# Kernel tuning notes

Hardware: AMD Instinct MI355X
Metric: run time of the kernel (lower is better)

Reference implementation:

```python
import jax, jax.numpy as jnp
import numpy as np

K = 64  # hardcoded in MAN.__init__
D_DRUG = 128
D_PROT = 128


def setup_inputs() -> dict:
    key = jax.random.key(0)
    ks = jax.random.split(key, 7)
    B, Ld, Lp = 64, 512, 1024

    def xavier(k, shape):
        fan_in, fan_out = shape[-1], shape[-2]
        std = (2.0 / (fan_in + fan_out)) ** 0.5
        return jax.random.normal(k, shape, dtype=jnp.float32) * std

    return {
        "drug": jax.random.normal(ks[0], (B, Ld, D_DRUG), dtype=jnp.float32),
        "target": jax.random.normal(ks[1], (B, Lp, D_PROT), dtype=jnp.float32),
        "W_b": xavier(ks[2], (D_PROT, D_DRUG)),
        "W_x": xavier(ks[3], (K, D_DRUG)),
        "W_p": xavier(ks[4], (K, D_PROT)),
        "w_hx": xavier(ks[5], (K, 1)),
        "w_hp": xavier(ks[6], (K, 1)),
    }


def reference(drug, target, W_b, W_x, W_p, w_hx, w_hp):
    # drug:   [B, Ld, Dd] ; target: [B, Lp, Dp]
    d = jnp.swapaxes(drug, 1, 2)            # [B, Dd, Ld]  (drug.permute(0,2,1))
    tT = jnp.swapaxes(target, 1, 2)         # [B, Dp, Lp]

    # C = tanh(target @ (W_b @ d))  -> [B, Lp, Ld]
    C = jnp.tanh(jnp.einsum('bpe,ed,bdl->bpl', target, W_b, d))

    Wx_d = jnp.einsum('kd,bdl->bkl', W_x, d)     # [B, k, Ld]
    Wp_t = jnp.einsum('ke,bep->bkp', W_p, tT)    # [B, k, Lp]

    H_c = jnp.tanh(Wx_d + jnp.einsum('bkp,bpl->bkl', Wp_t, C))   # [B, k, Ld]
    H_p = jnp.tanh(Wp_t + jnp.einsum('bkl,bpl->bkp', Wx_d, C))   # [B, k, Lp]

    a_c = jax.nn.softmax(jnp.einsum('k,bkl->bl', w_hx[:, 0], H_c), axis=-1)  # [B, Ld]
    a_p = jax.nn.softmax(jnp.einsum('k,bkp->bp', w_hp[:, 0], H_p), axis=-1)  # [B, Lp]

    c = jnp.einsum('bl,bld->bd', a_c, drug)      # [B, Dd]
    p = jnp.einsum('bp,bpe->be', a_p, target)    # [B, Dp]
    return (c, p)
```

## Files before the change

### kernel.cpp

```cpp
#include <hip/hip_runtime.h>
#include <hip/hip_bf16.h>
#include <math.h>

#define NB 64
#define LD 512
#define LP 1024
#define DD 128
#define KK 64

using half8 = __attribute__((ext_vector_type(8))) _Float16;
using half4 = __attribute__((ext_vector_type(4))) _Float16;
using f32x4 = __attribute__((ext_vector_type(4))) float;

__device__ __forceinline__ float ftanh(float x) {
    float e = __expf(2.0f * x);
    return 1.0f - 2.0f * __builtin_amdgcn_rcpf(e + 1.0f);
}

__global__ void k_conv(const float* __restrict__ in, _Float16* __restrict__ out, int n) {
    int i = (blockIdx.x * blockDim.x + threadIdx.x) * 4;
    int stride = gridDim.x * blockDim.x * 4;
    for (; i < n; i += stride) {
        float4 v = *reinterpret_cast<const float4*>(in + i);
        half4 h;
        h.x = (_Float16)v.x; h.y = (_Float16)v.y; h.z = (_Float16)v.z; h.w = (_Float16)v.w;
        *reinterpret_cast<half4*>(out + i) = h;
    }
}

__global__ void k_prep(const float* __restrict__ Wb, _Float16* __restrict__ WbT,
                       const float* __restrict__ Wx, _Float16* __restrict__ Wx_h,
                       const float* __restrict__ Wp, _Float16* __restrict__ Wp_h)
{
    int bid = blockIdx.x, tid = threadIdx.x;
    if (bid < 64) {
        int t = bid * 256 + tid;
        int d = t >> 7, e = t & 127;
        WbT[t] = (_Float16)Wb[e * 128 + d];
    } else {
        const float* src = (bid < 72) ? Wx : Wp;
        _Float16* dst = (bid < 72) ? Wx_h : Wp_h;
        int i = ((bid & 7) * 256 + tid) * 4;
        float4 v = *reinterpret_cast<const float4*>(src + i);
        half4 h;
        h.x = (_Float16)v.x; h.y = (_Float16)v.y; h.z = (_Float16)v.z; h.w = (_Float16)v.w;
        *reinterpret_cast<half4*>(dst + i) = h;
    }
}

__global__ void k_sentinel(float* out) {
    if (threadIdx.x == 0 && blockIdx.x == 0) out[0] = 1000.0f;
}

__global__ __launch_bounds__(256)
void k_gemm3(const _Float16* __restrict__ drug_h, const _Float16* __restrict__ targ_h,
             const _Float16* __restrict__ WbT_h, const _Float16* __restrict__ Wx_h,
             const _Float16* __restrict__ Wp_h,
             _Float16* __restrict__ tb_h, _Float16* __restrict__ Wxd_h,
             _Float16* __restrict__ Wpt_h)
{
    __shared__ alignas(16) _Float16 smem[64 * 72 + 128 * 72];
    _Float16* As = smem;
    _Float16* Bs = smem + 64 * 72;

    int bid = blockIdx.x;
    const _Float16 *A, *Bm;
    _Float16* Out;
    long sA, sB, sOut;
    int N, tilesN, t;
    const int Kd = 128;
    if (bid < 256)      { A = Wx_h;  sA = 0;            Bm = drug_h; sB = (long)LD * DD; Out = Wxd_h; sOut = (long)KK * LD; N = LD;  tilesN = 4; t = bid; }
    else if (bid < 768) { A = Wp_h;  sA = 0;            Bm = targ_h; sB = (long)LP * DD; Out = Wpt_h; sOut = (long)KK * LP; N = LP;  tilesN = 8; t = bid - 256; }
    else                { A = targ_h; sA = (long)LP * DD; Bm = WbT_h; sB = 0;            Out = tb_h;  sOut = (long)LP * DD; N = 128; tilesN = 1; t = bid - 768; }

    int tpb = (tilesN == 1) ? 16 : tilesN;
    int b = t / tpb;
    int q = t % tpb;
    int m0 = (tilesN == 1) ? q * 64 : 0;
    int n0 = (tilesN == 1) ? 0 : q * 128;

    const _Float16* Ab = A + (long)b * sA;
    const _Float16* Bb = Bm + (long)b * sB;

    int tid = threadIdx.x;
    int lane = tid & 63;
    int wid = tid >> 6;
    int wm = wid & 1, wn = wid >> 1;

    f32x4 acc[2][4];
#pragma unroll
    for (int i = 0; i < 2; i++)
#pragma unroll
        for (int j = 0; j < 4; j++) acc[i][j] = (f32x4)(0.0f);

    for (int k0 = 0; k0 < Kd; k0 += 64) {
#pragma unroll
        for (int i = 0; i < 2; i++) {
            int c = tid + i * 256;
            int row = c >> 3, col = c & 7;
            int4 v = *reinterpret_cast<const int4*>(Ab + (long)(m0 + row) * Kd + k0 + col * 8);
            *reinterpret_cast<int4*>(&As[row * 72 + col * 8]) = v;
        }
#pragma unroll
        for (int i = 0; i < 4; i++) {
            int c = tid + i * 256;
            int row = c >> 3, col = c & 7;
            int4 v = *reinterpret_cast<const int4*>(Bb + (long)(n0 + row) * Kd + k0 + col * 8);
            *reinterpret_cast<int4*>(&Bs[row * 72 + col * 8]) = v;
        }
        __syncthreads();
#pragma unroll
        for (int kk = 0; kk < 64; kk += 32) {
            int klane = kk + 8 * (lane >> 4);
            half8 af[2], bfr[4];
#pragma unroll
            for (int fm = 0; fm < 2; fm++)
                af[fm] = *reinterpret_cast<const half8*>(&As[(wm * 32 + fm * 16 + (lane & 15)) * 72 + klane]);
#pragma unroll
            for (int fn = 0; fn < 4; fn++)
                bfr[fn] = *reinterpret_cast<const half8*>(&Bs[(wn * 64 + fn * 16 + (lane & 15)) * 72 + klane]);
#pragma unroll
            for (int fm = 0; fm < 2; fm++)
#pragma unroll
                for (int fn = 0; fn < 4; fn++)
                    acc[fm][fn] = __builtin_amdgcn_mfma_f32_16x16x32_f16(af[fm], bfr[fn], acc[fm][fn], 0, 0, 0);
        }
        __syncthreads();
    }

    long ob = (long)b * sOut;
#pragma unroll
    for (int fm = 0; fm < 2; fm++)
#pragma unroll
        for (int fn = 0; fn < 4; fn++)
#pragma unroll
            for (int r = 0; r < 4; r++) {
                int row = m0 + wm * 32 + fm * 16 + (lane >> 4) * 4 + r;
                int col = n0 + wn * 64 + fn * 16 + (lane & 15);
                Out[ob + (long)row * N + col] = (_Float16)acc[fm][fn][r];
            }
}

__global__ __launch_bounds__(256, 3)
void k_score_fused(const _Float16* __restrict__ drug_h, const _Float16* __restrict__ tb_h,
                   const _Float16* __restrict__ Wxd_h, const _Float16* __restrict__ Wpt_h,
                   const float* __restrict__ whx, const float* __restrict__ whp,
                   float* __restrict__ sc_c, float* __restrict__ sc_p)
{
    __shared__ alignas(16) _Float16 Ss[64 * 136];
    __shared__ alignas(16) _Float16 Ws[64 * 72];
    __shared__ alignas(16) _Float16 Cts[128 * 72];
    __shared__ float sred[8 * 128];
    __shared__ float wsh[64];

    int P = blockIdx.x;
    int tid = threadIdx.x;
    int lane = tid & 63;
    int wid = tid >> 6;
    int wm = wid & 1, wn = wid >> 1;

    int b, n0, nsteps, Ntot, sW;
    const _Float16 *R, *S, *W, *Add;
    const float* wv;
    float* out;
    if (P < 256) {
        int x = P & 7, j = P >> 3;
        b = x * 8 + (j >> 2);
        n0 = (j & 3) * 128;
        R = drug_h + (long)b * (LD * DD);
        S = tb_h   + (long)b * (LP * DD);
        W = Wpt_h  + (long)b * (KK * LP);  sW = LP;
        Add = Wxd_h + (long)b * (KK * LD); Ntot = LD;
        nsteps = LP / 64; wv = whx; out = sc_c + (long)b * LD;
    } else {
        int Q = P - 256;
        int x = Q & 7, j = Q >> 3;
        b = x * 8 + (j >> 3);
        n0 = (j & 7) * 128;
        R = tb_h   + (long)b * (LP * DD);
        S = drug_h + (long)b * (LD * DD);
        W = Wxd_h  + (long)b * (KK * LD);  sW = LD;
        Add = Wpt_h + (long)b * (KK * LP); Ntot = LP;
        nsteps = LD / 64; wv = whp; out = sc_p + (long)b * LP;
    }

    half8 af[4][4];
#pragma unroll
    for (int fm = 0; fm < 4; fm++)
#pragma unroll
        for (int kk = 0; kk < 4; kk++) {
            int row = n0 + wm * 64 + fm * 16 + (lane & 15);
            int col = kk * 32 + 8 * (lane >> 4);
            af[fm][kk] = *reinterpret_cast<const half8*>(R + (long)row * DD + col);
        }
    if (tid < 64) wsh[tid] = wv[tid];

    f32x4 acc2[2][4];
#pragma unroll
    for (int i = 0; i < 2; i++)
#pragma unroll
        for (int j = 0; j < 4; j++) acc2[i][j] = (f32x4)(0.0f);

    for (int s = 0; s < nsteps; s++) {
        __syncthreads();
#pragma unroll
        for (int i = 0; i < 4; i++) {
            int c = tid + i * 256;
            int row = c >> 4, col8 = (c & 15) * 8;
            int4 v = *reinterpret_cast<const int4*>(S + (long)(s * 64 + row) * DD + col8);
            *reinterpret_cast<int4*>(&Ss[row * 136 + col8]) = v;
        }
#pragma unroll
        for (int i = 0; i < 2; i++) {
            int c = tid + i * 256;
            int row = c >> 3, col8 = (c & 7) * 8;
            int4 v = *reinterpret_cast<const int4*>(W + (long)row * sW + s * 64 + col8);
            *reinterpret_cast<int4*>(&Ws[row * 72 + col8]) = v;
        }
        __syncthreads();

        f32x4 a1[2][4];
#pragma unroll
        for (int i = 0; i < 2; i++)
#pragma unroll
            for (int j = 0; j < 4; j++) a1[i][j] = (f32x4)(0.0f);
#pragma unroll
        for (int kk = 0; kk < 4; kk++) {
            int klane = kk * 32 + 8 * (lane >> 4);
            half8 bf[2];
#pragma unroll
            for (int fn = 0; fn < 2; fn++)
                bf[fn] = *reinterpret_cast<const half8*>(&Ss[(wn * 32 + fn * 16 + (lane & 15)) * 136 + klane]);
#pragma unroll
            for (int fn = 0; fn < 2; fn++)
#pragma unroll
                for (int fm = 0; fm < 4; fm++)
                    a1[fn][fm] = __builtin_amdgcn_mfma_f32_16x16x32_f16(bf[fn], af[fm][kk], a1[fn][fm], 0, 0, 0);
        }
#pragma unroll
        for (int fn = 0; fn < 2; fn++)
#pragma unroll
            for (int fm = 0; fm < 4; fm++) {
                int res   = wm * 64 + fm * 16 + (lane & 15);
                int strm0 = wn * 32 + fn * 16 + 4 * (lane >> 4);
                half4 hv;
                hv.x = (_Float16)ftanh(a1[fn][fm][0]);
                hv.y = (_Float16)ftanh(a1[fn][fm][1]);
                hv.z = (_Float16)ftanh(a1[fn][fm][2]);
                hv.w = (_Float16)ftanh(a1[fn][fm][3]);
                *reinterpret_cast<half4*>(&Cts[res * 72 + strm0]) = hv;
            }
        __syncthreads();

#pragma unroll
        for (int kk = 0; kk < 2; kk++) {
            int klane = kk * 32 + 8 * (lane >> 4);
            half8 aw[2], bf2[4];
#pragma unroll
            for (int fm2 = 0; fm2 < 2; fm2++)
                aw[fm2] = *reinterpret_cast<const half8*>(&Ws[(wm * 32 + fm2 * 16 + (lane & 15)) * 72 + klane]);
#pragma unroll
            for (int fn2 = 0; fn2 < 4; fn2++)
                bf2[fn2] = *reinterpret_cast<const half8*>(&Cts[(wn * 64 + fn2 * 16 + (lane & 15)) * 72 + klane]);
#pragma unroll
            for (int fm2 = 0; fm2 < 2; fm2++)
#pragma unroll
                for (int fn2 = 0; fn2 < 4; fn2++)
                    acc2[fm2][fn2] = __builtin_amdgcn_mfma_f32_16x16x32_f16(aw[fm2], bf2[fn2], acc2[fm2][fn2], 0, 0, 0);
        }
    }

    float ps[4] = {0.f, 0.f, 0.f, 0.f};
#pragma unroll
    for (int fm2 = 0; fm2 < 2; fm2++)
#pragma unroll
        for (int fn2 = 0; fn2 < 4; fn2++)
#pragma unroll
            for (int r = 0; r < 4; r++) {
                int k   = wm * 32 + fm2 * 16 + (lane >> 4) * 4 + r;
                int col = wn * 64 + fn2 * 16 + (lane & 15);
                float v = ftanh(acc2[fm2][fn2][r] + (float)Add[(long)k * Ntot + n0 + col]);
                ps[fn2] += wsh[k] * v;
            }
#pragma unroll
    for (int fn2 = 0; fn2 < 4; fn2++)
        sred[(wm * 4 + (lane >> 4)) * 128 + wn * 64 + fn2 * 16 + (lane & 15)] = ps[fn2];
    __syncthreads();
    if (tid < 128) {
        float sacc = 0.f;
#pragma unroll
        for (int j = 0; j < 8; j++) sacc += sred[j * 128 + tid];
        out[n0 + tid] = sacc;
    }
}

__device__ __forceinline__ float wred_max(float v) {
#pragma unroll
    for (int off = 32; off > 0; off >>= 1) v = fmaxf(v, __shfl_xor(v, off, 64));
    return v;
}
__device__ __forceinline__ float wred_sum(float v) {
#pragma unroll
    for (int off = 32; off > 0; off >>= 1) v += __shfl_xor(v, off, 64);
    return v;
}

__global__ __launch_bounds__(1024)
void k_soft(const float* __restrict__ scc, const float* __restrict__ scp,
            float* __restrict__ ac, float* __restrict__ ap)
{
    __shared__ float r16[16];
    int b = blockIdx.x, tid = threadIdx.x;
    int lane = tid & 63, wid = tid >> 6;

    float s = (tid < 512) ? scc[b * 512 + tid] : -3.4e38f;
    float m = wred_max(s);
    if (lane == 0) r16[wid] = m;
    __syncthreads();
    m = r16[0];
#pragma unroll
    for (int i = 1; i < 16; i++) m = fmaxf(m, r16[i]);
    float e = (tid < 512) ? __expf(s - m) : 0.f;
    __syncthreads();
    float t = wred_sum(e);
    if (lane == 0) r16[wid] = t;
    __syncthreads();
    float sum = 0.f;
#pragma unroll
    for (int i = 0; i < 16; i++) sum += r16[i];
    if (tid < 512) ac[b * 512 + tid] = e * __builtin_amdgcn_rcpf(sum);
    __syncthreads();

    float s2 = scp[b * 1024 + tid];
    float m2 = wred_max(s2);
    if (lane == 0) r16[wid] = m2;
    __syncthreads();
    m2 = r16[0];
#pragma unroll
    for (int i = 1; i < 16; i++) m2 = fmaxf(m2, r16[i]);
    float e2 = __expf(s2 - m2);
    __syncthreads();
    float t2 = wred_sum(e2);
    if (lane == 0) r16[wid] = t2;
    __syncthreads();
    float sum2 = 0.f;
#pragma unroll
    for (int i = 0; i < 16; i++) sum2 += r16[i];
    ap[b * 1024 + tid] = e2 * __builtin_amdgcn_rcpf(sum2);
}

__global__ __launch_bounds__(512)
void k_wsum(const _Float16* __restrict__ drug_h, const _Float16* __restrict__ targ_h,
            const float* __restrict__ ac, const float* __restrict__ ap,
            float* __restrict__ out)
{
    __shared__ float ash[1024];
    __shared__ float red[32 * 128];
    int b = blockIdx.x, side = blockIdx.y;
    int L = side ? LP : LD;
    const _Float16* X = side ? targ_h : drug_h;
    const float* a = side ? ap : ac;
    float* ob = out + side * 8192 + b * 128;
    int tid = threadIdx.x;

    for (int i = tid; i < L; i += 512) ash[i] = a[(long)b * L + i];
    __syncthreads();

    int col8 = tid & 15, rg = tid >> 4;
    float accv[8];
#pragma unroll
    for (int j = 0; j < 8; j++) accv[j] = 0.f;
    const _Float16* Xb = X + (long)b * L * 128;
    for (int l = rg; l < L; l += 32) {
        half8 v = *reinterpret_cast<const half8*>(&Xb[l * 128 + col8 * 8]);
        float av = ash[l];
#pragma unroll
        for (int j = 0; j < 8; j++) accv[j] += av * (float)v[j];
    }
#pragma unroll
    for (int j = 0; j < 8; j++) red[rg * 128 + col8 * 8 + j] = accv[j];
    __syncthreads();
    if (tid < 128) {
        float s = 0.f;
#pragma unroll
        for (int g = 0; g < 32; g++) s += red[g * 128 + tid];
        ob[tid] = s;
    }
}

extern "C" void kernel_launch(void* const* d_in, const int* in_sizes, int n_in,
                              void* d_out, int out_size, void* d_ws, size_t ws_size,
                              hipStream_t stream) {
    (void)in_sizes; (void)n_in; (void)out_size;
    const float* drug   = (const float*)d_in[0];
    const float* target = (const float*)d_in[1];
    const float* Wb     = (const float*)d_in[2];
    const float* Wx     = (const float*)d_in[3];
    const float* Wp     = (const float*)d_in[4];
    const float* whx    = (const float*)d_in[5];
    const float* whp    = (const float*)d_in[6];

    char* w = (char*)d_ws;
    size_t off = 0;
    auto takeb = [&](size_t bytes) {
        void* p = (void*)(w + off);
        off += (bytes + 255) & ~(size_t)255;
        return p;
    };
    _Float16* drug_h = (_Float16*)takeb((size_t)NB * LD * DD * 2);
    _Float16* targ_h = (_Float16*)takeb((size_t)NB * LP * DD * 2);
    _Float16* WbT_h  = (_Float16*)takeb(128 * 128 * 2);
    _Float16* Wx_h   = (_Float16*)takeb(64 * 128 * 2);
    _Float16* Wp_h   = (_Float16*)takeb(64 * 128 * 2);
    _Float16* tb_h   = (_Float16*)takeb((size_t)NB * LP * DD * 2);
    _Float16* Wxd_h  = (_Float16*)takeb((size_t)NB * KK * LD * 2);
    _Float16* Wpt_h  = (_Float16*)takeb((size_t)NB * KK * LP * 2);
    float*    sc_c   = (float*)takeb((size_t)NB * LD * 4);
    float*    sc_p   = (float*)takeb((size_t)NB * LP * 4);
    float*    a_c    = (float*)takeb((size_t)NB * LD * 4);
    float*    a_p    = (float*)takeb((size_t)NB * LP * 4);

    if (off > ws_size) {
        k_sentinel<<<1, 64, 0, stream>>>((float*)d_out);
        return;
    }

    k_conv<<<1024, 256, 0, stream>>>(drug,   drug_h, NB * LD * DD);
    k_conv<<<1024, 256, 0, stream>>>(target, targ_h, NB * LP * DD);
    k_prep<<<80, 256, 0, stream>>>(Wb, WbT_h, Wx, Wx_h, Wp, Wp_h);

    k_gemm3<<<dim3(1792), 256, 0, stream>>>(
        drug_h, targ_h, WbT_h, Wx_h, Wp_h, tb_h, Wxd_h, Wpt_h);

    k_score_fused<<<dim3(256 + 512), 256, 0, stream>>>(
        drug_h, tb_h, Wxd_h, Wpt_h, whx, whp, sc_c, sc_p);

    k_soft<<<NB, 1024, 0, stream>>>(sc_c, sc_p, a_c, a_p);
    k_wsum<<<dim3(NB, 2), 512, 0, stream>>>(drug_h, targ_h, a_c, a_p, (float*)d_out);
}
```

Before: 87.84 us.

## Merge conversion/prep launches and register-prefetch next tile in score kernel

The two fp32-to-fp16 conversion kernels and the weight prep kernel are merged into one launch, cutting two kernel launches and their tail gaps. The fused score kernel now prefetches the next step's S and W tiles into registers right after the barrier, so global loads overlap with the MFMA work of the current step instead of stalling before it. The cost is extra registers per thread for the prefetch buffers, which could lower occupancy.

```diff
diff --git a/kernel.cpp b/kernel.cpp
--- a/kernel.cpp
+++ b/kernel.cpp
@@ -17,39 +17,44 @@
     return 1.0f - 2.0f * __builtin_amdgcn_rcpf(e + 1.0f);
 }
 
-__global__ void k_conv(const float* __restrict__ in, _Float16* __restrict__ out, int n) {
-    int i = (blockIdx.x * blockDim.x + threadIdx.x) * 4;
-    int stride = gridDim.x * blockDim.x * 4;
-    for (; i < n; i += stride) {
-        float4 v = *reinterpret_cast<const float4*>(in + i);
-        half4 h;
-        h.x = (_Float16)v.x; h.y = (_Float16)v.y; h.z = (_Float16)v.z; h.w = (_Float16)v.w;
-        *reinterpret_cast<half4*>(out + i) = h;
-    }
-}
-
-__global__ void k_prep(const float* __restrict__ Wb, _Float16* __restrict__ WbT,
-                       const float* __restrict__ Wx, _Float16* __restrict__ Wx_h,
-                       const float* __restrict__ Wp, _Float16* __restrict__ Wp_h)
+__global__ void k_sentinel(float* out) {
+    if (threadIdx.x == 0 && blockIdx.x == 0) out[0] = 1000.0f;
+}
+
+__global__ void k_convprep(const float* __restrict__ drug, _Float16* __restrict__ drug_h,
+                           const float* __restrict__ targ, _Float16* __restrict__ targ_h,
+                           const float* __restrict__ Wb, _Float16* __restrict__ WbT,
+                           const float* __restrict__ Wx, _Float16* __restrict__ Wx_h,
+                           const float* __restrict__ Wp, _Float16* __restrict__ Wp_h)
 {
     int bid = blockIdx.x, tid = threadIdx.x;
-    if (bid < 64) {
-        int t = bid * 256 + tid;
+    if (bid < 2048) {
+        const float* in = (bid < 1024) ? drug : targ;
+        _Float16* out = (bid < 1024) ? drug_h : targ_h;
+        int n = (bid < 1024) ? (NB * LD * DD) : (NB * LP * DD);
+        int blk = bid & 1023;
+        int i = (blk * 256 + tid) * 4;
+        int stride = 1024 * 256 * 4;
+        for (; i < n; i += stride) {
+            float4 v = *reinterpret_cast<const float4*>(in + i);
+            half4 h;
+            h.x = (_Float16)v.x; h.y = (_Float16)v.y; h.z = (_Float16)v.z; h.w = (_Float16)v.w;
+            *reinterpret_cast<half4*>(out + i) = h;
+        }
+    } else if (bid < 2112) {
+        int t = (bid - 2048) * 256 + tid;
         int d = t >> 7, e = t & 127;
         WbT[t] = (_Float16)Wb[e * 128 + d];
     } else {
-        const float* src = (bid < 72) ? Wx : Wp;
-        _Float16* dst = (bid < 72) ? Wx_h : Wp_h;
-        int i = ((bid & 7) * 256 + tid) * 4;
+        int q = bid - 2112;
+        const float* src = (q < 8) ? Wx : Wp;
+        _Float16* dst = (q < 8) ? Wx_h : Wp_h;
+        int i = ((q & 7) * 256 + tid) * 4;
         float4 v = *reinterpret_cast<const float4*>(src + i);
         half4 h;
         h.x = (_Float16)v.x; h.y = (_Float16)v.y; h.z = (_Float16)v.z; h.w = (_Float16)v.w;
         *reinterpret_cast<half4*>(dst + i) = h;
     }
-}
-
-__global__ void k_sentinel(float* out) {
-    if (threadIdx.x == 0 && blockIdx.x == 0) out[0] = 1000.0f;
 }
 
 __global__ __launch_bounds__(256)
@@ -195,6 +200,18 @@
         }
     if (tid < 64) wsh[tid] = wv[tid];
 
+    int rS = tid >> 4, cS = (tid & 15) * 8;
+    int rW = tid >> 3, cW = (tid & 7) * 8;
+    int4 s0_, s1_, s2_, s3_, w0_, w1_;
+    {
+        s0_ = *reinterpret_cast<const int4*>(S + (long)(rS)      * DD + cS);
+        s1_ = *reinterpret_cast<const int4*>(S + (long)(rS + 16) * DD + cS);
+        s2_ = *reinterpret_cast<const int4*>(S + (long)(rS + 32) * DD + cS);
+        s3_ = *reinterpret_cast<const int4*>(S + (long)(rS + 48) * DD + cS);
+        w0_ = *reinterpret_cast<const int4*>(W + (long)(rW)      * sW + cW);
+        w1_ = *reinterpret_cast<const int4*>(W + (long)(rW + 32) * sW + cW);
+    }
+
     f32x4 acc2[2][4];
 #pragma unroll
     for (int i = 0; i < 2; i++)
@@ -203,21 +220,22 @@
 
     for (int s = 0; s < nsteps; s++) {
         __syncthreads();
-#pragma unroll
-        for (int i = 0; i < 4; i++) {
-            int c = tid + i * 256;
-            int row = c >> 4, col8 = (c & 15) * 8;
-            int4 v = *reinterpret_cast<const int4*>(S + (long)(s * 64 + row) * DD + col8);
-            *reinterpret_cast<int4*>(&Ss[row * 136 + col8]) = v;
-        }
-#pragma unroll
-        for (int i = 0; i < 2; i++) {
-            int c = tid + i * 256;
-            int row = c >> 3, col8 = (c & 7) * 8;
-            int4 v = *reinterpret_cast<const int4*>(W + (long)row * sW + s * 64 + col8);
-            *reinterpret_cast<int4*>(&Ws[row * 72 + col8]) = v;
-        }
+        *reinterpret_cast<int4*>(&Ss[(rS)      * 136 + cS]) = s0_;
+        *reinterpret_cast<int4*>(&Ss[(rS + 16) * 136 + cS]) = s1_;
+        *reinterpret_cast<int4*>(&Ss[(rS + 32) * 136 + cS]) = s2_;
+        *reinterpret_cast<int4*>(&Ss[(rS + 48) * 136 + cS]) = s3_;
+        *reinterpret_cast<int4*>(&Ws[(rW)      * 72 + cW]) = w0_;
+        *reinterpret_cast<int4*>(&Ws[(rW + 32) * 72 + cW]) = w1_;
         __syncthreads();
+        if (s + 1 < nsteps) {
+            int s1n = (s + 1) * 64;
+            s0_ = *reinterpret_cast<const int4*>(S + (long)(s1n + rS)      * DD + cS);
+            s1_ = *reinterpret_cast<const int4*>(S + (long)(s1n + rS + 16) * DD + cS);
+            s2_ = *reinterpret_cast<const int4*>(S + (long)(s1n + rS + 32) * DD + cS);
+            s3_ = *reinterpret_cast<const int4*>(S + (long)(s1n + rS + 48) * DD + cS);
+            w0_ = *reinterpret_cast<const int4*>(W + (long)(rW)      * sW + s1n + cW);
+            w1_ = *reinterpret_cast<const int4*>(W + (long)(rW + 32) * sW + s1n + cW);
+        }
 
         f32x4 a1[2][4];
 #pragma unroll
@@ -425,9 +443,8 @@
         return;
     }
 
-    k_conv<<<1024, 256, 0, stream>>>(drug,   drug_h, NB * LD * DD);
-    k_conv<<<1024, 256, 0, stream>>>(target, targ_h, NB * LP * DD);
-    k_prep<<<80, 256, 0, stream>>>(Wb, WbT_h, Wx, Wx_h, Wp, Wp_h);
+    k_convprep<<<2128, 256, 0, stream>>>(drug, drug_h, target, targ_h,
+                                         Wb, WbT_h, Wx, Wx_h, Wp, Wp_h);
 
     k_gemm3<<<dim3(1792), 256, 0, stream>>>(
         drug_h, targ_h, WbT_h, Wx_h, Wp_h, tb_h, Wxd_h, Wpt_h);
```

Result: faster. 83.89 us (-4.5%).
